# Optimization experiments

Measured on AMD Instinct MI355X. Metric: run time of the kernel, lower is better.

Reference implementation:

```python
import jax, jax.numpy as jnp
import numpy as np

N, B, OBS, ACT = 8, 32768, 128, 32
E, H = 128, 4
D = E // H  # attend_dim = 32
EPS = 1e-5


def setup_inputs() -> dict:
    key = jax.random.key(0)
    ks = jax.random.split(key, 20)
    sc = np.float32(0.02)
    inp = {
        "observation_vector": jax.random.normal(ks[0], (N, B, OBS), jnp.float32),
        "action_vector": jax.random.normal(ks[1], (N, B, ACT), jnp.float32),
        # per-agent BatchNorm affine params (training-mode batch stats are used)
        "bn_g_gamma": jnp.ones((N, OBS + ACT), jnp.float32),
        "bn_g_beta": jnp.zeros((N, OBS + ACT), jnp.float32),
        "bn_s_gamma": jnp.ones((N, OBS), jnp.float32),
        "bn_s_beta": jnp.zeros((N, OBS), jnp.float32),
        # per-agent g / state-only Linear layers
        "g_w": jax.random.normal(ks[2], (N, E, OBS + ACT), jnp.float32) * sc,
        "g_b": jnp.zeros((N, E), jnp.float32),
        "s_w": jax.random.normal(ks[3], (N, E, OBS), jnp.float32) * sc,
        "s_b": jnp.zeros((N, E), jnp.float32),
        # per-head attention projections (no bias)
        "wq": jax.random.normal(ks[4], (H, D, E), jnp.float32) * sc,
        "wk": jax.random.normal(ks[5], (H, D, E), jnp.float32) * sc,
        "wv": jax.random.normal(ks[6], (H, D, E), jnp.float32) * sc,
        # per-agent f networks: Linear(E + H*D -> E), Linear(E -> ACT)
        "f1_w": jax.random.normal(ks[7], (N, E, E + H * D), jnp.float32) * sc,
        "f1_b": jnp.zeros((N, E), jnp.float32),
        "f2_w": jax.random.normal(ks[8], (N, ACT, E), jnp.float32) * sc,
        "f2_b": jnp.zeros((N, ACT), jnp.float32),
    }
    return inp


def _bn(x, gamma, beta):
    # x: [N, B, F]; training-mode BatchNorm1d per agent (biased variance)
    mu = x.mean(axis=1, keepdims=True)
    var = x.var(axis=1, keepdims=True)
    return (x - mu) / jnp.sqrt(var + EPS) * gamma[:, None, :] + beta[:, None, :]


def _lrelu(x):
    return jax.nn.leaky_relu(x, 0.01)


def reference(observation_vector, action_vector, bn_g_gamma, bn_g_beta, bn_s_gamma,
              bn_s_beta, g_w, g_b, s_w, s_b, wq, wk, wv, f1_w, f1_b, f2_w, f2_b):
    obs, act = observation_vector, action_vector
    ga = jnp.concatenate([obs, act], axis=-1)                       # [N,B,OBS+ACT]
    e = _lrelu(jnp.einsum('nbf,nef->nbe', _bn(ga, bn_g_gamma, bn_g_beta), g_w)
               + g_b[:, None, :])                                   # [N,B,E]
    s = _lrelu(jnp.einsum('nbf,nef->nbe', _bn(obs, bn_s_gamma, bn_s_beta), s_w)
               + s_b[:, None, :])                                   # [N,B,E]
    q = jnp.einsum('nbe,hde->hnbd', e, wq)                          # [H,N,B,D]
    k = jnp.einsum('nbe,hde->hnbd', e, wk)
    v = _lrelu(jnp.einsum('nbe,hde->hnbd', e, wv))
    # leave-one-out attention over agents: mask the diagonal (self)
    logits = jnp.einsum('hnbd,hmbd->hbnm', q, k) / jnp.sqrt(jnp.float32(D))
    logits = jnp.where(jnp.eye(N, dtype=bool), -jnp.inf, logits)
    alpha = jax.nn.softmax(logits, axis=-1)                         # [H,B,N,N]
    xi = jnp.einsum('hbnm,hmbd->nbhd', alpha, v)                    # [N,B,H,D]
    xi = xi.reshape(N, xi.shape[1], H * D)
    fin = jnp.concatenate([xi, s], axis=-1)                         # [N,B,H*D+E]
    h1 = _lrelu(jnp.einsum('nbf,nef->nbe', fin, f1_w) + f1_b[:, None, :])
    all_q = jnp.einsum('nbe,nae->nba', h1, f2_w) + f2_b[:, None, :]  # [N,B,ACT]
    ids = jnp.argmax(act, axis=-1, keepdims=True)                   # [N,B,1]
    curr_q = jnp.take_along_axis(all_q, ids, axis=-1)               # [N,B,1]
    return curr_q
```

## Files before the change

kernel.cpp:

```cpp
#include <hip/hip_runtime.h>

#define N_AG 8
#define BTOT 32768
#define OBSF 128
#define ACTF 32
#define CHUNK 8192
#define NCH 4
#define HH 4

#define WS_STATS   0u
#define WS_SCALES  (16u<<10)
#define WS_BIASES  (48u<<10)
#define WS_WQKV    (64u<<10)
#define WS_F2W     (160u<<10)
#define WS_F1W     (224u<<10)
#define WS_WG      (768u<<10)
#define WS_IDS     (1536u<<10)
#define WS_ES      (4u<<20)
#define WS_XI      (40u<<20)
#define WS_NEED    ((size_t)60<<20)

typedef __attribute__((ext_vector_type(8))) __bf16 bf16x8;
typedef __attribute__((ext_vector_type(8))) short short8;
typedef __attribute__((ext_vector_type(4))) float f32x4;

static __device__ __forceinline__ unsigned short f2bf(float f){
  unsigned u = __builtin_bit_cast(unsigned, f);
  u += 0x7fffu + ((u >> 16) & 1u);
  return (unsigned short)(u >> 16);
}
static __device__ __forceinline__ bf16x8 ldb8(const unsigned short* p){
  return __builtin_bit_cast(bf16x8, *(const short8*)p);
}
static __device__ __forceinline__ f32x4 mfma16(bf16x8 a, bf16x8 b, f32x4 c){
  return __builtin_amdgcn_mfma_f32_16x16x32_bf16(a, b, c, 0, 0, 0);
}

__global__ void k_zero(float* stats){
  for (int i = threadIdx.x; i < 2560; i += 256) stats[i] = 0.f;
}

__global__ __launch_bounds__(256) void k_stats_obs(const float* __restrict__ obs,
                                                   float* __restrict__ stats){
  int n = blockIdx.y, ch = blockIdx.x;
  int c = threadIdx.x & 31, r = threadIdx.x >> 5;
  const float4* p = (const float4*)(obs + ((size_t)n*BTOT + (size_t)ch*256 + r)*OBSF) + c;
  float sx=0.f, sy=0.f, sz=0.f, sw=0.f;
  float qx=0.f, qy=0.f, qz=0.f, qw=0.f;
  #pragma unroll 4
  for (int i = 0; i < 32; i++){
    float4 v = p[(size_t)i*8*(OBSF/4)];
    sx += v.x; sy += v.y; sz += v.z; sw += v.w;
    qx += v.x*v.x; qy += v.y*v.y; qz += v.z*v.z; qw += v.w*v.w;
  }
  __shared__ float4 rs[8][32], rq[8][32];
  rs[r][c] = make_float4(sx, sy, sz, sw);
  rq[r][c] = make_float4(qx, qy, qz, qw);
  __syncthreads();
  if (threadIdx.x < 128){
    int f = threadIdx.x;
    float ss = 0.f, qq = 0.f;
    #pragma unroll
    for (int g = 0; g < 8; g++){
      ss += ((const float*)&rs[g][f>>2])[f&3];
      qq += ((const float*)&rq[g][f>>2])[f&3];
    }
    atomicAdd(&stats[n*128 + f], ss);
    atomicAdd(&stats[1024 + n*128 + f], qq);
  }
}

__global__ __launch_bounds__(256) void k_stats_act(const float* __restrict__ act,
                                                   float* __restrict__ stats,
                                                   int* __restrict__ ids){
  int n = blockIdx.y, ch = blockIdx.x;
  int c = threadIdx.x & 7, r = threadIdx.x >> 3;
  int f0 = c*4;
  float sx=0.f, sy=0.f, sz=0.f, sw=0.f;
  float qx=0.f, qy=0.f, qz=0.f, qw=0.f;
  #pragma unroll
  for (int i = 0; i < 4; i++){
    int b = ch*128 + i*32 + r;
    float4 v = *(const float4*)(act + ((size_t)n*BTOT + b)*ACTF + f0);
    sx += v.x; sy += v.y; sz += v.z; sw += v.w;
    qx += v.x*v.x; qy += v.y*v.y; qz += v.z*v.z; qw += v.w*v.w;
    float mv = v.x; int mi = f0;
    if (v.y > mv){ mv = v.y; mi = f0+1; }
    if (v.z > mv){ mv = v.z; mi = f0+2; }
    if (v.w > mv){ mv = v.w; mi = f0+3; }
    #pragma unroll
    for (int m = 1; m <= 4; m <<= 1){
      float ov = __shfl_xor(mv, m);
      int   oi = __shfl_xor(mi, m);
      if (ov > mv || (ov == mv && oi < mi)){ mv = ov; mi = oi; }
    }
    if (c == 0) ids[(size_t)n*BTOT + b] = mi;
  }
  __shared__ float4 rs[32][8], rq[32][8];
  rs[r][c] = make_float4(sx, sy, sz, sw);
  rq[r][c] = make_float4(qx, qy, qz, qw);
  __syncthreads();
  if (threadIdx.x < 32){
    int f = threadIdx.x;
    float ss = 0.f, qq = 0.f;
    #pragma unroll
    for (int g = 0; g < 32; g++){
      ss += ((const float*)&rs[g][f>>2])[f&3];
      qq += ((const float*)&rq[g][f>>2])[f&3];
    }
    atomicAdd(&stats[2048 + n*32 + f], ss);
    atomicAdd(&stats[2304 + n*32 + f], qq);
  }
}

__global__ void k_finalize(const float* __restrict__ stats, const float* __restrict__ gg,
                           const float* __restrict__ gb, const float* __restrict__ sg,
                           const float* __restrict__ sb, float* __restrict__ scales){
  int n = blockIdx.x, f = threadIdx.x;
  if (f < 160){
    float mu, va;
    if (f < 128){ mu = stats[n*128+f] * (1.f/BTOT); va = stats[1024+n*128+f]*(1.f/BTOT) - mu*mu; }
    else { int fa = f-128; mu = stats[2048+n*32+fa]*(1.f/BTOT); va = stats[2304+n*32+fa]*(1.f/BTOT) - mu*mu; }
    float inv = 1.f / sqrtf(va + 1e-5f);
    float a = gg[n*160+f] * inv;
    scales[n*160+f] = a;
    scales[1280 + n*160+f] = gb[n*160+f] - mu*a;
    if (f < 128){
      float a2 = sg[n*128+f] * inv;
      scales[2560 + n*128+f] = a2;
      scales[3584 + n*128+f] = sb[n*128+f] - mu*a2;
    }
  }
}

__global__ void k_fold(const float* __restrict__ g_w, const float* __restrict__ g_b,
                       const float* __restrict__ s_w, const float* __restrict__ s_b,
                       const float* __restrict__ wq, const float* __restrict__ wk,
                       const float* __restrict__ wv, const float* __restrict__ f1w_in,
                       const float* __restrict__ f2w_in, const float* __restrict__ scales,
                       unsigned short* __restrict__ wg, float* __restrict__ bias_es,
                       unsigned short* __restrict__ wqkv, unsigned short* __restrict__ f1w,
                       unsigned short* __restrict__ f2w){
  int blk = blockIdx.x, t = threadIdx.x;
  if (blk < 2048){
    int n = blk >> 8, o = blk & 255;
    float part = 0.f;
    if (t < 160){
      float w, a, c;
      if (o < 128){ w = g_w[((size_t)n*128 + o)*160 + t]; a = scales[n*160+t]; c = scales[1280+n*160+t]; }
      else if (t < 128){ w = s_w[((size_t)n*128 + (o-128))*128 + t]; a = scales[2560+n*128+t]; c = scales[3584+n*128+t]; }
      else { w = 0.f; a = 0.f; c = 0.f; }
      wg[((size_t)n*256 + o)*160 + t] = f2bf(w*a);
      part = w * c;
    }
    __shared__ float red[256];
    red[t] = part; __syncthreads();
    for (int s2 = 128; s2 > 0; s2 >>= 1){ if (t < s2) red[t] += red[t+s2]; __syncthreads(); }
    if (t == 0){
      float base = (o < 128) ? g_b[n*128+o] : s_b[n*128+(o-128)];
      bias_es[n*256+o] = base + red[0];
    }
  } else if (blk < 2240){
    int idx = (blk-2048)*256 + t;
    int r = idx >> 7, f = idx & 127, rr = r & 127;
    const float* src = (r < 128) ? wq : (r < 256 ? wk : wv);
    wqkv[idx] = f2bf(src[rr*128 + f]);
  } else if (blk < 3264){
    int idx = (blk-2240)*256 + t;
    f1w[idx] = f2bf(f1w_in[idx]);
  } else {
    int idx = (blk-3264)*256 + t;
    f2w[idx] = f2bf(f2w_in[idx]);
  }
}

__global__ __launch_bounds__(256) void k_gemm_es(const float* __restrict__ obs,
    const float* __restrict__ act, const unsigned short* __restrict__ wg,
    const float* __restrict__ biases, unsigned short* __restrict__ es, int chunk){
  int n = blockIdx.y, mbb = blockIdx.x;
  int tid = threadIdx.x, w = tid >> 6, l = tid & 63, lr = l & 15, lg = l >> 4;
  __shared__ unsigned short wsm[256*160];
  {
    const int4* src = (const int4*)(wg + (size_t)n*(256*160));
    int4* dst = (int4*)wsm;
    for (int i = tid; i < 256*160/8; i += 256) dst[i] = src[i];
  }
  int brow = mbb*128 + w*16 + lr;
  size_t bglob = (size_t)n*BTOT + (size_t)chunk*CHUNK + brow;
  float4 x0[10];
  #pragma unroll
  for (int kt = 0; kt < 4; kt++){
    const float4* pa = (const float4*)(obs + bglob*OBSF + kt*32 + lg*8);
    x0[kt*2] = pa[0]; x0[kt*2+1] = pa[1];
  }
  { const float4* pa = (const float4*)(act + bglob*ACTF + lg*8);
    x0[8] = pa[0]; x0[9] = pa[1]; }
  __syncthreads();
  f32x4 zero = {0.f,0.f,0.f,0.f};
  bf16x8 af[5];
  #pragma unroll
  for (int kt = 0; kt < 5; kt++){
    float4 a = x0[kt*2], b = x0[kt*2+1];
    af[kt][0]=(__bf16)a.x; af[kt][1]=(__bf16)a.y; af[kt][2]=(__bf16)a.z; af[kt][3]=(__bf16)a.w;
    af[kt][4]=(__bf16)b.x; af[kt][5]=(__bf16)b.y; af[kt][6]=(__bf16)b.z; af[kt][7]=(__bf16)b.w;
  }
  float4 x1[10];
  #pragma unroll
  for (int kt = 0; kt < 4; kt++){
    const float4* pa = (const float4*)(obs + (bglob+64)*OBSF + kt*32 + lg*8);
    x1[kt*2] = pa[0]; x1[kt*2+1] = pa[1];
  }
  { const float4* pa = (const float4*)(act + (bglob+64)*ACTF + lg*8);
    x1[8] = pa[0]; x1[9] = pa[1]; }
  f32x4 acc[16];
  #pragma unroll
  for (int i = 0; i < 16; i++) acc[i] = zero;
  #pragma unroll
  for (int kt = 0; kt < 5; kt++)
    #pragma unroll
    for (int nt = 0; nt < 16; nt++){
      bf16x8 bf = ldb8(&wsm[(nt*16 + lr)*160 + kt*32 + lg*8]);
      acc[nt] = mfma16(af[kt], bf, acc[nt]);
    }
  #pragma unroll
  for (int nt = 0; nt < 16; nt++){
    int col = nt*16 + lr;
    float bias = biases[n*256 + col];
    #pragma unroll
    for (int r = 0; r < 4; r++){
      float v = acc[nt][r] + bias;
      v = v > 0.f ? v : 0.01f*v;
      int orow = mbb*128 + w*16 + lg*4 + r;
      es[((size_t)n*CHUNK + orow)*256 + col] = f2bf(v);
    }
  }
  #pragma unroll
  for (int kt = 0; kt < 5; kt++){
    float4 a = x1[kt*2], b = x1[kt*2+1];
    af[kt][0]=(__bf16)a.x; af[kt][1]=(__bf16)a.y; af[kt][2]=(__bf16)a.z; af[kt][3]=(__bf16)a.w;
    af[kt][4]=(__bf16)b.x; af[kt][5]=(__bf16)b.y; af[kt][6]=(__bf16)b.z; af[kt][7]=(__bf16)b.w;
  }
  #pragma unroll
  for (int i = 0; i < 16; i++) acc[i] = zero;
  #pragma unroll
  for (int kt = 0; kt < 5; kt++)
    #pragma unroll
    for (int nt = 0; nt < 16; nt++){
      bf16x8 bf = ldb8(&wsm[(nt*16 + lr)*160 + kt*32 + lg*8]);
      acc[nt] = mfma16(af[kt], bf, acc[nt]);
    }
  #pragma unroll
  for (int nt = 0; nt < 16; nt++){
    int col = nt*16 + lr;
    float bias = biases[n*256 + col];
    #pragma unroll
    for (int r = 0; r < 4; r++){
      float v = acc[nt][r] + bias;
      v = v > 0.f ? v : 0.01f*v;
      int orow = mbb*128 + 64 + w*16 + lg*4 + r;
      es[((size_t)n*CHUNK + orow)*256 + col] = f2bf(v);
    }
  }
}

__global__ __launch_bounds__(256) void k_attn(const unsigned short* __restrict__ es,
    const unsigned short* __restrict__ wqkv, unsigned short* __restrict__ xi, int chunk){
  int bt = blockIdx.x;
  int tid = threadIdx.x, w = tid >> 6, l = tid & 63, lr = l & 15, lg = l >> 4;
  __shared__ unsigned short eT[128][136];
  __shared__ unsigned short qkvT[128][104];
  for (int i = tid; i < 128*16; i += 256){
    int row = i >> 4, c = (i & 15)*8;
    *(int4*)&eT[row][c] =
      *(const int4*)&es[((size_t)(row>>4)*CHUNK + bt*16 + (row&15))*256 + c];
  }
  __syncthreads();
  for (int h = 0; h < HH; h++){
    f32x4 zero = {0.f,0.f,0.f,0.f};
    f32x4 acc[2][6];
    #pragma unroll
    for (int mt = 0; mt < 2; mt++)
      #pragma unroll
      for (int nt = 0; nt < 6; nt++) acc[mt][nt] = zero;
    #pragma unroll
    for (int kt = 0; kt < 4; kt++){
      int f0 = kt*32 + lg*8;
      bf16x8 a0 = ldb8(&eT[w*32 + lr][f0]);
      bf16x8 a1 = ldb8(&eT[w*32 + 16 + lr][f0]);
      #pragma unroll
      for (int nt = 0; nt < 6; nt++){
        int r = nt*16 + lr, sec = r >> 5, j = r & 31;
        bf16x8 bf = ldb8(&wqkv[((size_t)sec*128 + h*32 + j)*128 + f0]);
        acc[0][nt] = mfma16(a0, bf, acc[0][nt]);
        acc[1][nt] = mfma16(a1, bf, acc[1][nt]);
      }
    }
    __syncthreads();
    #pragma unroll
    for (int mt = 0; mt < 2; mt++)
      #pragma unroll
      for (int nt = 0; nt < 6; nt++)
        #pragma unroll
        for (int r = 0; r < 4; r++){
          float v = acc[mt][nt][r];
          if (nt >= 4) v = v > 0.f ? v : 0.01f*v;
          qkvT[w*32 + mt*16 + lg*4 + r][nt*16 + lr] = f2bf(v);
        }
    __syncthreads();
    {
      int dh = tid & 1, bi = (tid >> 1) & 15, nq = tid >> 5;
      int rq = nq*16 + bi;
      float qv[16];
      { bf16x8 t0 = ldb8(&qkvT[rq][dh*16]);
        bf16x8 t1 = ldb8(&qkvT[rq][dh*16 + 8]);
        #pragma unroll
        for (int i = 0; i < 8; i++){ qv[i] = (float)t0[i]; qv[8+i] = (float)t1[i]; } }
      float lgt[8];
      #pragma unroll
      for (int m = 0; m < 8; m++){
        bf16x8 k0 = ldb8(&qkvT[m*16+bi][32 + dh*16]);
        bf16x8 k1 = ldb8(&qkvT[m*16+bi][32 + dh*16 + 8]);
        float d = 0.f;
        #pragma unroll
        for (int i = 0; i < 8; i++){ d += qv[i]*(float)k0[i]; d += qv[8+i]*(float)k1[i]; }
        d += __shfl_xor(d, 1);
        lgt[m] = d * 0.17677669529663687f;
      }
      float mx = -1e30f;
      #pragma unroll
      for (int m = 0; m < 8; m++) if (m != nq) mx = fmaxf(mx, lgt[m]);
      float p[8], sum = 0.f;
      #pragma unroll
      for (int m = 0; m < 8; m++){ p[m] = (m == nq) ? 0.f : __expf(lgt[m] - mx); sum += p[m]; }
      float inv = 1.f / sum;
      float xa[16];
      #pragma unroll
      for (int i = 0; i < 16; i++) xa[i] = 0.f;
      #pragma unroll
      for (int m = 0; m < 8; m++){
        float al = p[m]*inv;
        bf16x8 v0 = ldb8(&qkvT[m*16+bi][64 + dh*16]);
        bf16x8 v1 = ldb8(&qkvT[m*16+bi][64 + dh*16 + 8]);
        #pragma unroll
        for (int i = 0; i < 8; i++){ xa[i] += al*(float)v0[i]; xa[8+i] += al*(float)v1[i]; }
      }
      short8 o0, o1;
      #pragma unroll
      for (int i = 0; i < 8; i++){ o0[i] = (short)f2bf(xa[i]); o1[i] = (short)f2bf(xa[8+i]); }
      size_t orow = (size_t)nq*CHUNK + bt*16 + bi;
      *(short8*)&xi[orow*128 + h*32 + dh*16]     = o0;
      *(short8*)&xi[orow*128 + h*32 + dh*16 + 8] = o1;
    }
  }
}

__global__ __launch_bounds__(256) void k_gemm_f(const unsigned short* __restrict__ xi,
    const unsigned short* __restrict__ es, const unsigned short* __restrict__ f1w,
    const float* __restrict__ f1b, const unsigned short* __restrict__ f2w,
    const float* __restrict__ f2b, const int* __restrict__ ids,
    float* __restrict__ out, int chunk){
  int n = blockIdx.y, mbb = blockIdx.x;
  int tid = threadIdx.x, w = tid >> 6, l = tid & 63, lr = l & 15, lg = l >> 4;
  __shared__ unsigned short f1T[128*264];
  __shared__ unsigned short f2T[32*136];
  __shared__ unsigned short h1T[64*136];
  __shared__ float allq[64*32];
  for (int i = tid; i < 128*32; i += 256){
    int r = i >> 5, c = (i & 31)*8;
    *(int4*)&f1T[r*264 + c] = *(const int4*)&f1w[((size_t)n*128 + r)*256 + c];
  }
  for (int i = tid; i < 32*16; i += 256){
    int r = i >> 4, c = (i & 15)*8;
    *(int4*)&f2T[r*136 + c] = *(const int4*)&f2w[((size_t)n*32 + r)*128 + c];
  }
  bf16x8 xf[2][8];
  {
    int arow0 = mbb*256 + w*16 + lr;
    #pragma unroll
    for (int kt = 0; kt < 4; kt++)
      xf[0][kt] = ldb8(&xi[((size_t)n*CHUNK + arow0)*128 + kt*32 + lg*8]);
    #pragma unroll
    for (int kt = 0; kt < 4; kt++)
      xf[0][4+kt] = ldb8(&es[((size_t)n*CHUNK + arow0)*256 + 128 + kt*32 + lg*8]);
  }
  __syncthreads();
  f32x4 zero = {0.f,0.f,0.f,0.f};
  #pragma unroll
  for (int sub = 0; sub < 4; sub++){
    const int cur = sub & 1, nxt = cur ^ 1;
    int mb = mbb*4 + sub;
    if (sub < 3){
      int arown = mb*64 + 64 + w*16 + lr;
      #pragma unroll
      for (int kt = 0; kt < 4; kt++)
        xf[nxt][kt] = ldb8(&xi[((size_t)n*CHUNK + arown)*128 + kt*32 + lg*8]);
      #pragma unroll
      for (int kt = 0; kt < 4; kt++)
        xf[nxt][4+kt] = ldb8(&es[((size_t)n*CHUNK + arown)*256 + 128 + kt*32 + lg*8]);
    }
    f32x4 a1[8];
    #pragma unroll
    for (int i = 0; i < 8; i++) a1[i] = zero;
    #pragma unroll
    for (int kt = 0; kt < 8; kt++)
      #pragma unroll
      for (int nt = 0; nt < 8; nt++){
        bf16x8 bf = ldb8(&f1T[(nt*16 + lr)*264 + kt*32 + lg*8]);
        a1[nt] = mfma16(xf[cur][kt], bf, a1[nt]);
      }
    #pragma unroll
    for (int nt = 0; nt < 8; nt++){
      int col = nt*16 + lr;
      float bias = f1b[n*128 + col];
      #pragma unroll
      for (int r = 0; r < 4; r++){
        float v = a1[nt][r] + bias;
        v = v > 0.f ? v : 0.01f*v;
        h1T[(w*16 + lg*4 + r)*136 + col] = f2bf(v);
      }
    }
    __syncthreads();
    f32x4 a2[2];
    a2[0] = zero; a2[1] = zero;
    #pragma unroll
    for (int kt = 0; kt < 4; kt++){
      int f0 = kt*32 + lg*8;
      bf16x8 hf = ldb8(&h1T[(w*16 + lr)*136 + f0]);
      #pragma unroll
      for (int nt = 0; nt < 2; nt++){
        bf16x8 bf = ldb8(&f2T[(nt*16 + lr)*136 + f0]);
        a2[nt] = mfma16(hf, bf, a2[nt]);
      }
    }
    #pragma unroll
    for (int nt = 0; nt < 2; nt++){
      int col = nt*16 + lr;
      float bias = f2b[n*32 + col];
      #pragma unroll
      for (int r = 0; r < 4; r++)
        allq[(w*16 + lg*4 + r)*32 + col] = a2[nt][r] + bias;
    }
    __syncthreads();
    if (tid < 64){
      size_t bglob = (size_t)chunk*CHUNK + mb*64 + tid;
      int id = ids[(size_t)n*BTOT + bglob];
      out[(size_t)n*BTOT + bglob] = allq[tid*32 + id];
    }
  }
}

extern "C" void kernel_launch(void* const* d_in, const int* in_sizes, int n_in,
                              void* d_out, int out_size, void* d_ws, size_t ws_size,
                              hipStream_t stream){
  if (ws_size < WS_NEED) return;
  const float* obs  = (const float*)d_in[0];
  const float* act  = (const float*)d_in[1];
  const float* gg   = (const float*)d_in[2];
  const float* gb   = (const float*)d_in[3];
  const float* sg   = (const float*)d_in[4];
  const float* sb   = (const float*)d_in[5];
  const float* g_w  = (const float*)d_in[6];
  const float* g_b  = (const float*)d_in[7];
  const float* s_w  = (const float*)d_in[8];
  const float* s_b  = (const float*)d_in[9];
  const float* wq   = (const float*)d_in[10];
  const float* wk   = (const float*)d_in[11];
  const float* wv   = (const float*)d_in[12];
  const float* f1w_in = (const float*)d_in[13];
  const float* f1b  = (const float*)d_in[14];
  const float* f2w_in = (const float*)d_in[15];
  const float* f2b  = (const float*)d_in[16];
  char* ws = (char*)d_ws;
  float* stats   = (float*)(ws + WS_STATS);
  float* scales  = (float*)(ws + WS_SCALES);
  float* bias_es = (float*)(ws + WS_BIASES);
  unsigned short* wqkv = (unsigned short*)(ws + WS_WQKV);
  unsigned short* f2wb = (unsigned short*)(ws + WS_F2W);
  unsigned short* f1wb = (unsigned short*)(ws + WS_F1W);
  unsigned short* wg   = (unsigned short*)(ws + WS_WG);
  int* ids             = (int*)(ws + WS_IDS);
  unsigned short* esb  = (unsigned short*)(ws + WS_ES);
  unsigned short* xib  = (unsigned short*)(ws + WS_XI);
  float* out = (float*)d_out;

  k_zero<<<1, 256, 0, stream>>>(stats);
  k_stats_obs<<<dim3(128,8), 256, 0, stream>>>(obs, stats);
  k_stats_act<<<dim3(256,8), 256, 0, stream>>>(act, stats, ids);
  k_finalize<<<8, 256, 0, stream>>>(stats, gg, gb, sg, sb, scales);
  k_fold<<<3392, 256, 0, stream>>>(g_w, g_b, s_w, s_b, wq, wk, wv, f1w_in, f2w_in,
                                   scales, wg, bias_es, wqkv, f1wb, f2wb);
  for (int c = 0; c < NCH; c++){
    k_gemm_es<<<dim3(64,8), 256, 0, stream>>>(obs, act, wg, bias_es, esb, c);
    k_attn<<<512, 256, 0, stream>>>(esb, wqkv, xib, c);
    k_gemm_f<<<dim3(32,8), 256, 0, stream>>>(xib, esb, f1wb, f1b, f2wb, f2b, ids, out, c);
  }
}
```

Baseline: 365.7 us.

## Process full batch in single launches instead of four chunked passes

Removes the four-way batch chunking loop so each of the three main kernels launches once over the whole batch, with larger es/xi workspace buffers sized for all rows. This cuts launch count and tail effects and gives each launch a bigger grid. The trade-off is that intermediates (about 128 MB of es plus 64 MB of xi) no longer fit in cache between stages, where a chunked pass could have kept them L2/LLC-resident.

```diff
diff --git a/kernel.cpp b/kernel.cpp
--- a/kernel.cpp
+++ b/kernel.cpp
@@ -4,8 +4,6 @@
 #define BTOT 32768
 #define OBSF 128
 #define ACTF 32
-#define CHUNK 8192
-#define NCH 4
 #define HH 4
 
 #define WS_STATS   0u
@@ -17,8 +15,8 @@
 #define WS_WG      (768u<<10)
 #define WS_IDS     (1536u<<10)
 #define WS_ES      (4u<<20)
-#define WS_XI      (40u<<20)
-#define WS_NEED    ((size_t)60<<20)
+#define WS_XI      (136u<<20)
+#define WS_NEED    ((size_t)200<<20)
 
 typedef __attribute__((ext_vector_type(8))) __bf16 bf16x8;
 typedef __attribute__((ext_vector_type(8))) short short8;
@@ -176,7 +174,7 @@
 
 __global__ __launch_bounds__(256) void k_gemm_es(const float* __restrict__ obs,
     const float* __restrict__ act, const unsigned short* __restrict__ wg,
-    const float* __restrict__ biases, unsigned short* __restrict__ es, int chunk){
+    const float* __restrict__ biases, unsigned short* __restrict__ es){
   int n = blockIdx.y, mbb = blockIdx.x;
   int tid = threadIdx.x, w = tid >> 6, l = tid & 63, lr = l & 15, lg = l >> 4;
   __shared__ unsigned short wsm[256*160];
@@ -186,7 +184,7 @@
     for (int i = tid; i < 256*160/8; i += 256) dst[i] = src[i];
   }
   int brow = mbb*128 + w*16 + lr;
-  size_t bglob = (size_t)n*BTOT + (size_t)chunk*CHUNK + brow;
+  size_t bglob = (size_t)n*BTOT + brow;
   float4 x0[10];
   #pragma unroll
   for (int kt = 0; kt < 4; kt++){
@@ -231,7 +229,7 @@
       float v = acc[nt][r] + bias;
       v = v > 0.f ? v : 0.01f*v;
       int orow = mbb*128 + w*16 + lg*4 + r;
-      es[((size_t)n*CHUNK + orow)*256 + col] = f2bf(v);
+      es[((size_t)n*BTOT + orow)*256 + col] = f2bf(v);
     }
   }
   #pragma unroll
@@ -258,13 +256,13 @@
       float v = acc[nt][r] + bias;
       v = v > 0.f ? v : 0.01f*v;
       int orow = mbb*128 + 64 + w*16 + lg*4 + r;
-      es[((size_t)n*CHUNK + orow)*256 + col] = f2bf(v);
+      es[((size_t)n*BTOT + orow)*256 + col] = f2bf(v);
     }
   }
 }
 
 __global__ __launch_bounds__(256) void k_attn(const unsigned short* __restrict__ es,
-    const unsigned short* __restrict__ wqkv, unsigned short* __restrict__ xi, int chunk){
+    const unsigned short* __restrict__ wqkv, unsigned short* __restrict__ xi){
   int bt = blockIdx.x;
   int tid = threadIdx.x, w = tid >> 6, l = tid & 63, lr = l & 15, lg = l >> 4;
   __shared__ unsigned short eT[128][136];
@@ -272,7 +270,7 @@
   for (int i = tid; i < 128*16; i += 256){
     int row = i >> 4, c = (i & 15)*8;
     *(int4*)&eT[row][c] =
-      *(const int4*)&es[((size_t)(row>>4)*CHUNK + bt*16 + (row&15))*256 + c];
+      *(const int4*)&es[((size_t)(row>>4)*BTOT + bt*16 + (row&15))*256 + c];
   }
   __syncthreads();
   for (int h = 0; h < HH; h++){
@@ -347,7 +345,7 @@
       short8 o0, o1;
       #pragma unroll
       for (int i = 0; i < 8; i++){ o0[i] = (short)f2bf(xa[i]); o1[i] = (short)f2bf(xa[8+i]); }
-      size_t orow = (size_t)nq*CHUNK + bt*16 + bi;
+      size_t orow = (size_t)nq*BTOT + bt*16 + bi;
       *(short8*)&xi[orow*128 + h*32 + dh*16]     = o0;
       *(short8*)&xi[orow*128 + h*32 + dh*16 + 8] = o1;
     }
@@ -358,7 +356,7 @@
     const unsigned short* __restrict__ es, const unsigned short* __restrict__ f1w,
     const float* __restrict__ f1b, const unsigned short* __restrict__ f2w,
     const float* __restrict__ f2b, const int* __restrict__ ids,
-    float* __restrict__ out, int chunk){
+    float* __restrict__ out){
   int n = blockIdx.y, mbb = blockIdx.x;
   int tid = threadIdx.x, w = tid >> 6, l = tid & 63, lr = l & 15, lg = l >> 4;
   __shared__ unsigned short f1T[128*264];
@@ -378,10 +376,10 @@
     int arow0 = mbb*256 + w*16 + lr;
     #pragma unroll
     for (int kt = 0; kt < 4; kt++)
-      xf[0][kt] = ldb8(&xi[((size_t)n*CHUNK + arow0)*128 + kt*32 + lg*8]);
+      xf[0][kt] = ldb8(&xi[((size_t)n*BTOT + arow0)*128 + kt*32 + lg*8]);
     #pragma unroll
     for (int kt = 0; kt < 4; kt++)
-      xf[0][4+kt] = ldb8(&es[((size_t)n*CHUNK + arow0)*256 + 128 + kt*32 + lg*8]);
+      xf[0][4+kt] = ldb8(&es[((size_t)n*BTOT + arow0)*256 + 128 + kt*32 + lg*8]);
   }
   __syncthreads();
   f32x4 zero = {0.f,0.f,0.f,0.f};
@@ -393,10 +391,10 @@
       int arown = mb*64 + 64 + w*16 + lr;
       #pragma unroll
       for (int kt = 0; kt < 4; kt++)
-        xf[nxt][kt] = ldb8(&xi[((size_t)n*CHUNK + arown)*128 + kt*32 + lg*8]);
+        xf[nxt][kt] = ldb8(&xi[((size_t)n*BTOT + arown)*128 + kt*32 + lg*8]);
       #pragma unroll
       for (int kt = 0; kt < 4; kt++)
-        xf[nxt][4+kt] = ldb8(&es[((size_t)n*CHUNK + arown)*256 + 128 + kt*32 + lg*8]);
+        xf[nxt][4+kt] = ldb8(&es[((size_t)n*BTOT + arown)*256 + 128 + kt*32 + lg*8]);
     }
     f32x4 a1[8];
     #pragma unroll
@@ -442,7 +440,7 @@
     }
     __syncthreads();
     if (tid < 64){
-      size_t bglob = (size_t)chunk*CHUNK + mb*64 + tid;
+      size_t bglob = (size_t)mb*64 + tid;
       int id = ids[(size_t)n*BTOT + bglob];
       out[(size_t)n*BTOT + bglob] = allq[tid*32 + id];
     }
@@ -489,9 +487,7 @@
   k_finalize<<<8, 256, 0, stream>>>(stats, gg, gb, sg, sb, scales);
   k_fold<<<3392, 256, 0, stream>>>(g_w, g_b, s_w, s_b, wq, wk, wv, f1w_in, f2w_in,
                                    scales, wg, bias_es, wqkv, f1wb, f2wb);
-  for (int c = 0; c < NCH; c++){
-    k_gemm_es<<<dim3(64,8), 256, 0, stream>>>(obs, act, wg, bias_es, esb, c);
-    k_attn<<<512, 256, 0, stream>>>(esb, wqkv, xib, c);
-    k_gemm_f<<<dim3(32,8), 256, 0, stream>>>(xib, esb, f1wb, f1b, f2wb, f2b, ids, out, c);
-  }
-}
+  k_gemm_es<<<dim3(256,8), 256, 0, stream>>>(obs, act, wg, bias_es, esb);
+  k_attn<<<2048, 256, 0, stream>>>(esb, wqkv, xib);
+  k_gemm_f<<<dim3(128,8), 256, 0, stream>>>(xib, esb, f1wb, f1b, f2wb, f2b, ids, out);
+}
```

New measurement: 374.0 us. +2.3%, slower.
